# Kernel optimization log

Hardware: AMD Instinct MI355X
Metric: run time of the kernel (lower is better)

The kernel has to match this reference:

```python
import jax, jax.numpy as jnp
import numpy as np

NEG_SLOPE = 0.2  # PyG GATConv default negative_slope
EPS = 1e-16     # PyG softmax denominator epsilon


def gat_layer(x, src, dst, W, att_src, att_dst, bias, N):
    """PyG-style GATConv: gather -> leaky-relu score -> segment softmax -> scatter-add.
    x: [N, F_in], W: [F_in, H*C], att_src/att_dst: [H, C], bias: [H*C].
    src/dst: [E] edge endpoints (messages flow src -> dst), self-loops included.
    """
    H, C = att_src.shape
    h = (x @ W).reshape(N, H, C)                       # [N, H, C]
    a_s = jnp.sum(h * att_src, axis=-1)                # [N, H]
    a_d = jnp.sum(h * att_dst, axis=-1)                # [N, H]
    e = a_s[src] + a_d[dst]                            # [E, H]
    e = jnp.where(e > 0, e, NEG_SLOPE * e)             # leaky relu
    m = jax.ops.segment_max(e, dst, num_segments=N)    # [N, H] (self-loops ensure every node hit)
    p = jnp.exp(e - m[dst])                            # [E, H]
    s = jax.ops.segment_sum(p, dst, num_segments=N)    # [N, H]
    alpha = p / (s[dst] + EPS)                         # [E, H]
    out = jax.ops.segment_sum(alpha[:, :, None] * h[src], dst, num_segments=N)  # [N, H, C]
    return out.reshape(N, H * C) + bias


def setup_inputs() -> dict:
    key = jax.random.key(0)
    ks = jax.random.split(key, 12)
    N, E = 100000, 1600000
    x = jax.random.normal(ks[0], (N, 1), dtype=jnp.float32)
    edge_index = jax.random.randint(ks[1], (2, E), 0, N, dtype=jnp.int32)
    sc = 0.1
    # conv1: in=1, heads=4, out=8
    W1 = jax.random.normal(ks[2], (1, 32), dtype=jnp.float32) * sc
    att_src1 = jax.random.normal(ks[3], (4, 8), dtype=jnp.float32) * sc
    att_dst1 = jax.random.normal(ks[4], (4, 8), dtype=jnp.float32) * sc
    bias1 = jnp.zeros((32,), dtype=jnp.float32)
    # conv2: in=32, heads=8, out=8
    W2 = jax.random.normal(ks[5], (32, 64), dtype=jnp.float32) * sc
    att_src2 = jax.random.normal(ks[6], (8, 8), dtype=jnp.float32) * sc
    att_dst2 = jax.random.normal(ks[7], (8, 8), dtype=jnp.float32) * sc
    bias2 = jnp.zeros((64,), dtype=jnp.float32)
    # fc2: 64 -> 1
    fc_w = jax.random.normal(ks[8], (64, 1), dtype=jnp.float32) * sc
    fc_b = jnp.zeros((1,), dtype=jnp.float32)
    return {"x": x, "edge_index": edge_index,
            "W1": W1, "att_src1": att_src1, "att_dst1": att_dst1, "bias1": bias1,
            "W2": W2, "att_src2": att_src2, "att_dst2": att_dst2, "bias2": bias2,
            "fc_w": fc_w, "fc_b": fc_b}


def reference(x, edge_index, W1, att_src1, att_dst1, bias1,
              W2, att_src2, att_dst2, bias2, fc_w, fc_b):
    N = x.shape[0]
    loop = jnp.arange(N, dtype=edge_index.dtype)       # add_self_loops=True (PyG default)
    src = jnp.concatenate([edge_index[0], loop])
    dst = jnp.concatenate([edge_index[1], loop])
    h = jax.nn.elu(gat_layer(x, src, dst, W1, att_src1, att_dst1, bias1, N))
    h = jax.nn.elu(gat_layer(h, src, dst, W2, att_src2, att_dst2, bias2, N))
    return h @ fc_w + fc_b                             # [N, 1]
```

## Files before the change

kernel.cpp:

```cpp
#include <hip/hip_runtime.h>
#include <hip/hip_fp16.h>
#include <cmath>

#define TPB 256
#define STPB 512
#define NSLOPE 0.2f
#define SEPS 1e-16f

#define BSH 7
#define BNODES 128
#define NBMAX 1024
#define NCHUNK2 256
#define SCTPB 1024
#define CAP 32
#define STAGE 4608
#define MAXDEG 96

__device__ __forceinline__ float lrelu(float v) { return v > 0.f ? v : NSLOPE * v; }
__device__ __forceinline__ float elu1(float v)  { return v > 0.f ? v : expm1f(v); }
__device__ __forceinline__ float elu1f(float v) { return v > 0.f ? v : __expf(v) - 1.f; }

__global__ void k_bscatter(const int* __restrict__ srcI, const int* __restrict__ dstI,
                           int E, int NB, int chunk,
                           int* __restrict__ pk, unsigned char* __restrict__ cnt8) {
    __shared__ int cntL[NBMAX];
    int t = threadIdx.x;
    int c = blockIdx.x;
    int beg = c * chunk;
    int end = min(beg + chunk, E);
    for (int i = t; i < NBMAX; i += SCTPB) cntL[i] = 0;
    __syncthreads();
    for (int e = beg + t; e < end; e += SCTPB) {
        int s = srcI[e], d = dstI[e];
        int b = d >> BSH;
        int r = atomicAdd(&cntL[b], 1);
        if (r < CAP)
            pk[((size_t)b * NCHUNK2 + c) * CAP + r] = (s << BSH) | (d & (BNODES - 1));
    }
    __syncthreads();
    for (int i = t; i < NB; i += SCTPB)
        cnt8[(size_t)i * NCHUNK2 + c] = (unsigned char)min(cntL[i], CAP);
}

__global__ void k_sl1h2(const int* __restrict__ pk, const unsigned char* __restrict__ cnt8,
                        unsigned cap,
                        const float* __restrict__ x,
                        const float* __restrict__ as1, const float* __restrict__ ad1,
                        const float* __restrict__ W1, const float* __restrict__ b1,
                        const float* __restrict__ W2, const float* __restrict__ attS,
                        const float* __restrict__ attD, int N,
                        unsigned* __restrict__ offsets, int* __restrict__ sortedSrc,
                        __half* __restrict__ h2h, float* __restrict__ aS, float* __restrict__ aD) {
    __shared__ __align__(16) char upool[BNODES * 36 * 4];
    int* praw = (int*)upool;
    float (*lds1)[36] = (float (*)[36])upool;
    __shared__ int sorted[STAGE];
    __shared__ int cnt[BNODES];
    __shared__ int offl[BNODES];
    __shared__ int scnt[NCHUNK2];
    __shared__ int sbase[NCHUNK2];
    __shared__ float SDs[8];
    __shared__ int wt4[4], wo4[4];
    __shared__ int mTot, w0tot;
    int b = blockIdx.x, t = threadIdx.x;
    int lane = t & 63, wv = t >> 6;
    int base = b << BSH;
    unsigned rbeg = (unsigned)b * cap;
    if (t < BNODES) cnt[t] = (base + t < N) ? 1 : 0;
    if (t < 8) {
        int h = t & 3;
        const float* att = (t >= 4) ? ad1 : as1;
        float acc = 0.f;
        #pragma unroll
        for (int cc = 0; cc < 8; ++cc) acc += W1[h*8+cc] * att[h*8+cc];
        SDs[t] = acc;
    }
    int myc = (t < NCHUNK2) ? (int)cnt8[(size_t)b * NCHUNK2 + t] : 0;
    int inc2 = myc;
    #pragma unroll
    for (int off = 1; off < 64; off <<= 1) {
        int u = __shfl_up(inc2, off);
        if (lane >= off) inc2 += u;
    }
    if (t < NCHUNK2 && lane == 63) wt4[wv] = inc2;
    __syncthreads();
    if (t < 4) {
        int xv = wt4[t];
        int sc_ = xv;
        #pragma unroll
        for (int off = 1; off < 4; off <<= 1) {
            int u = __shfl_up(sc_, off);
            if (t >= off) sc_ += u;
        }
        wo4[t] = sc_ - xv;
        if (t == 3) mTot = sc_;
    }
    __syncthreads();
    if (t < NCHUNK2) {
        scnt[t] = myc;
        sbase[t] = inc2 + wo4[wv] - myc;
    }
    __syncthreads();
    {
        const int4* slab = (const int4*)(pk + (size_t)b * NCHUNK2 * CAP);
        for (int i4 = t; i4 < NCHUNK2 * CAP / 4; i4 += STPB) {
            int4 v = slab[i4];
            int c = i4 >> 3;
            int j0 = (i4 & 7) << 2;
            int cv = scnt[c];
            if (j0 < cv) {
                int sb = sbase[c];
                int nv = min(4, cv - j0);
                int vv0 = v.x, vv1 = v.y, vv2 = v.z, vv3 = v.w;
                if (0 < nv && sb + j0 + 0 < STAGE) { praw[sb + j0 + 0] = vv0; atomicAdd(&cnt[vv0 & (BNODES - 1)], 1); }
                if (1 < nv && sb + j0 + 1 < STAGE) { praw[sb + j0 + 1] = vv1; atomicAdd(&cnt[vv1 & (BNODES - 1)], 1); }
                if (2 < nv && sb + j0 + 2 < STAGE) { praw[sb + j0 + 2] = vv2; atomicAdd(&cnt[vv2 & (BNODES - 1)], 1); }
                if (3 < nv && sb + j0 + 3 < STAGE) { praw[sb + j0 + 3] = vv3; atomicAdd(&cnt[vv3 & (BNODES - 1)], 1); }
            }
        }
        if (t < BNODES && base + t < N && mTot + t < STAGE)
            praw[mTot + t] = ((base + t) << BSH) | t;
    }
    __syncthreads();
    int m = min(mTot + min(BNODES, N - base), STAGE);
    int v = (t < BNODES) ? cnt[t] : 0;
    int inc = v;
    #pragma unroll
    for (int off = 1; off < 64; off <<= 1) {
        int u = __shfl_up(inc, off);
        if (lane >= off) inc += u;
    }
    if (t == 63) w0tot = inc;
    __syncthreads();
    if (t >= 64 && t < BNODES) inc += w0tot;
    if (t < BNODES) {
        int ex = inc - v;
        int d = base + t;
        if (d < N) offsets[d] = ((rbeg + (unsigned)ex) << 10) | (unsigned)v;
        cnt[t] = 0;
        offl[t] = ex;
    }
    __syncthreads();
    for (int i = t; i < m; i += STPB) {
        int p = praw[i];
        int dl = p & (BNODES - 1);
        int r = atomicAdd(&cnt[dl], 1);
        sorted[offl[dl] + r] = p >> BSH;
    }
    __syncthreads();
    for (int i = t; i < m; i += STPB) sortedSrc[rbeg + i] = sorted[i];
    __syncthreads();
    int n = t >> 2, q = t & 3;
    int d2 = base + n;
    bool active = (d2 < N);
    float s0 = 0.f, s1 = 0.f, s2 = 0.f, s3 = 0.f;
    float g0 = 0.f, g1 = 0.f, g2 = 0.f, g3 = 0.f;
    if (active) {
        int deg = cnt[n];
        int lbeg = offl[n];
        float xd = x[d2];
        float S0 = SDs[0], S1 = SDs[1], S2 = SDs[2], S3 = SDs[3];
        float D0 = xd*SDs[4], D1 = xd*SDs[5], D2 = xd*SDs[6], D3 = xd*SDs[7];
        int dq = (deg + 3) >> 2;
        int i = lbeg + q * dq;
        int rem = min(dq, deg - q * dq);
        for (; rem >= 2; rem -= 2, i += 2) {
            int a0 = sorted[i];
            int a1 = sorted[i + 1];
            float x0 = x[a0], x1 = x[a1];
            float p;
            p = __expf(lrelu(x0*S0 + D0)); s0 += p; g0 += p * x0;
            p = __expf(lrelu(x0*S1 + D1)); s1 += p; g1 += p * x0;
            p = __expf(lrelu(x0*S2 + D2)); s2 += p; g2 += p * x0;
            p = __expf(lrelu(x0*S3 + D3)); s3 += p; g3 += p * x0;
            p = __expf(lrelu(x1*S0 + D0)); s0 += p; g0 += p * x1;
            p = __expf(lrelu(x1*S1 + D1)); s1 += p; g1 += p * x1;
            p = __expf(lrelu(x1*S2 + D2)); s2 += p; g2 += p * x1;
            p = __expf(lrelu(x1*S3 + D3)); s3 += p; g3 += p * x1;
        }
        if (rem > 0) {
            int a0 = sorted[i];
            float xs = x[a0];
            float p;
            p = __expf(lrelu(xs*S0 + D0)); s0 += p; g0 += p * xs;
            p = __expf(lrelu(xs*S1 + D1)); s1 += p; g1 += p * xs;
            p = __expf(lrelu(xs*S2 + D2)); s2 += p; g2 += p * xs;
            p = __expf(lrelu(xs*S3 + D3)); s3 += p; g3 += p * xs;
        }
    }
    s0 += __shfl_xor(s0, 1); s1 += __shfl_xor(s1, 1);
    s2 += __shfl_xor(s2, 1); s3 += __shfl_xor(s3, 1);
    g0 += __shfl_xor(g0, 1); g1 += __shfl_xor(g1, 1);
    g2 += __shfl_xor(g2, 1); g3 += __shfl_xor(g3, 1);
    s0 += __shfl_xor(s0, 2); s1 += __shfl_xor(s1, 2);
    s2 += __shfl_xor(s2, 2); s3 += __shfl_xor(s3, 2);
    g0 += __shfl_xor(g0, 2); g1 += __shfl_xor(g1, 2);
    g2 += __shfl_xor(g2, 2); g3 += __shfl_xor(g3, 2);
    if (active) {
        float gq = (q == 0) ? g0 / (s0 + SEPS) :
                   (q == 1) ? g1 / (s1 + SEPS) :
                   (q == 2) ? g2 / (s2 + SEPS) :
                              g3 / (s3 + SEPS);
        #pragma unroll
        for (int cc = 0; cc < 8; ++cc)
            lds1[n][q*8+cc] = elu1(gq * W1[q*8+cc] + b1[q*8+cc]);
    }
    __syncthreads();
    int sub = t >> 6;
    float w2r[32];
    #pragma unroll
    for (int k = 0; k < 32; ++k) w2r[k] = W2[k*64 + lane];
    float attSl = attS[lane], attDl = attD[lane];
    int nCnt = min(BNODES, N - base);
    for (int nn = sub; nn < nCnt; nn += 8) {
        const float4* row4 = (const float4*)lds1[nn];
        float acc = 0.f;
        #pragma unroll
        for (int k4 = 0; k4 < 8; ++k4) {
            float4 rv = row4[k4];
            acc += rv.x*w2r[4*k4] + rv.y*w2r[4*k4+1] + rv.z*w2r[4*k4+2] + rv.w*w2r[4*k4+3];
        }
        int node = base + nn;
        h2h[(size_t)node*64 + lane] = __float2half(acc);
        float ps = acc * attSl;
        float pd = acc * attDl;
        #pragma unroll
        for (int mm = 1; mm < 8; mm <<= 1) {
            ps += __shfl_xor(ps, mm);
            pd += __shfl_xor(pd, mm);
        }
        int hh = lane >> 3, cc = lane & 7;
        if (cc == 0) aS[(size_t)node*8 + hh] = ps;
        if (cc == 1) aD[(size_t)node*8 + hh] = pd;
    }
}

__global__ void k_agg(const unsigned* __restrict__ offsets, const int* __restrict__ ss,
                      const float* __restrict__ aS, const float* __restrict__ aD,
                      const __half* __restrict__ h2h, const float* __restrict__ b2,
                      const float* __restrict__ fcw, const float* __restrict__ fcb,
                      float* __restrict__ out, int N) {
    __shared__ int sl[4][MAXDEG];
    int lane = threadIdx.x & 63;
    int w = threadIdx.x >> 6;
    int d = blockIdx.x * 4 + w;
    if (d >= N) return;
    unsigned u = offsets[d];
    unsigned beg = u >> 10;
    int deg = (int)(u & 1023u);
    int lH   = lane & 31;
    int half = lane >> 5;
    int hh   = lH >> 2;
    const __half2* __restrict__ hp = (const __half2*)h2h;
    float sum = 0.f, ax = 0.f, ay = 0.f;
    if (deg <= MAXDEG) {
        int degPad = (deg + 7) & ~7;
        for (int j = lane; j < degPad; j += 64) sl[w][j] = ss[beg + (unsigned)min(j, deg - 1)];
        float adv = aD[(unsigned)d * 8u + (unsigned)hh];
        for (int e = 0; e < degPad; e += 8) {
            int bi = e + half;
            int s0 = sl[w][bi],     s1 = sl[w][bi + 2];
            int s2 = sl[w][bi + 4], s3 = sl[w][bi + 6];
            float a0 = aS[(unsigned)s0 * 8u + (unsigned)hh];
            float a1 = aS[(unsigned)s1 * 8u + (unsigned)hh];
            float a2 = aS[(unsigned)s2 * 8u + (unsigned)hh];
            float a3 = aS[(unsigned)s3 * 8u + (unsigned)hh];
            float2 g0 = __half22float2(hp[(unsigned)s0 * 32u + (unsigned)lH]);
            float2 g1 = __half22float2(hp[(unsigned)s1 * 32u + (unsigned)lH]);
            float2 g2 = __half22float2(hp[(unsigned)s2 * 32u + (unsigned)lH]);
            float2 g3 = __half22float2(hp[(unsigned)s3 * 32u + (unsigned)lH]);
            float p0 = __expf(lrelu(a0 + adv));
            float p1 = __expf(lrelu(a1 + adv));
            float p2 = __expf(lrelu(a2 + adv));
            float p3 = __expf(lrelu(a3 + adv));
            if (e + 8 > deg) {
                if (bi     >= deg) p0 = 0.f;
                if (bi + 2 >= deg) p1 = 0.f;
                if (bi + 4 >= deg) p2 = 0.f;
                if (bi + 6 >= deg) p3 = 0.f;
            }
            ax += p0*g0.x + p1*g1.x + p2*g2.x + p3*g3.x;
            ay += p0*g0.y + p1*g1.y + p2*g2.y + p3*g3.y;
            sum += (p0 + p1) + (p2 + p3);
        }
    } else {
        float adh = aD[(size_t)d*8 + hh];
        for (int e = half; e < deg; e += 2) {
            int s = ss[beg + e];
            float p = __expf(lrelu(aS[(size_t)s*8 + hh] + adh));
            float2 g = __half22float2(*(const __half2*)(h2h + (size_t)s*64 + 2*lH));
            ax += p*g.x; ay += p*g.y; sum += p;
        }
    }
    ax  += __shfl_xor(ax, 32);
    ay  += __shfl_xor(ay, 32);
    sum += __shfl_xor(sum, 32);
    float inv = 1.f / (sum + SEPS);
    float tt = elu1f(ax*inv + b2[2*lH]) * fcw[2*lH]
             + elu1f(ay*inv + b2[2*lH+1]) * fcw[2*lH+1];
    #pragma unroll
    for (int m = 16; m; m >>= 1) tt += __shfl_xor(tt, m);
    if (lane == 0) out[d] = tt + fcb[0];
}

extern "C" void kernel_launch(void* const* d_in, const int* in_sizes, int n_in,
                              void* d_out, int out_size, void* d_ws, size_t ws_size,
                              hipStream_t stream) {
    const float* x    = (const float*)d_in[0];
    const int*   ei   = (const int*)  d_in[1];
    const float* W1   = (const float*)d_in[2];
    const float* as1  = (const float*)d_in[3];
    const float* ad1  = (const float*)d_in[4];
    const float* b1   = (const float*)d_in[5];
    const float* W2   = (const float*)d_in[6];
    const float* attS2= (const float*)d_in[7];
    const float* attD2= (const float*)d_in[8];
    const float* b2   = (const float*)d_in[9];
    const float* fcw  = (const float*)d_in[10];
    const float* fcb  = (const float*)d_in[11];
    float* out = (float*)d_out;

    int N = in_sizes[0];
    int E = in_sizes[1] / 2;
    int ET = E + N;
    int NB = (N + BNODES - 1) / BNODES;
    unsigned cap = (unsigned)((ET + NB - 1) / NB + 512);
    cap = (cap + 3u) & ~3u;

    const int* srcI = ei;
    const int* dstI = ei + E;

    float* ws = (float*)d_ws;
    size_t off = 0;
    int*      pk        = (int*)(ws + off); off += (size_t)NB * NCHUNK2 * CAP;
    unsigned char* cnt8 = (unsigned char*)(ws + off); off += ((size_t)NB * NCHUNK2 + 3) / 4;
    unsigned* offsets   = (unsigned*)(ws + off); off += (size_t)N + 16;
    int*      sortedSrc = (int*)(ws + off); off += (size_t)NB * cap;
    float*    aS2       = ws + off; off += (size_t)N * 8;
    float*    aD2       = ws + off; off += (size_t)N * 8;
    off = (off + 31) & ~(size_t)31;
    __half*   h2h       = (__half*)(ws + off); off += (size_t)N * 32;

    int chunk = (E + NCHUNK2 - 1) / NCHUNK2;
    k_bscatter<<<NCHUNK2, SCTPB, 0, stream>>>(srcI, dstI, E, NB, chunk, pk, cnt8);
    k_sl1h2   <<<NB, STPB, 0, stream>>>(pk, cnt8, cap, x, as1, ad1, W1, b1,
                                        W2, attS2, attD2,
                                        N, offsets, sortedSrc, h2h, aS2, aD2);
    k_agg     <<<(N + 3) / 4, TPB, 0, stream>>>(offsets, sortedSrc, aS2, aD2, h2h,
                                                b2, fcw, fcb, out, N);
}
```

Before: 188.0 us.

## Split fused sort and layer-1/h2 kernel into separate sort and compute kernels

The fused bucket-sort plus layer-1 aggregation plus h2 projection kernel becomes two kernels. k_sort builds offsets and the sorted source list. k_l1h2 then reads them back from global memory, with 64 nodes per 256-thread block. The split aims to shrink the large LDS footprint and register pressure so the compute phase reaches higher occupancy and more blocks. The cost is an extra launch and a global round trip of sortedSrc instead of reading it from LDS.

```diff
diff --git a/kernel.cpp b/kernel.cpp
--- a/kernel.cpp
+++ b/kernel.cpp
@@ -14,6 +14,7 @@
 #define SCTPB 1024
 #define CAP 32
 #define STAGE 4608
+#define LNODES 64
 #define MAXDEG 96
 
 __device__ __forceinline__ float lrelu(float v) { return v > 0.f ? v : NSLOPE * v; }
@@ -42,24 +43,15 @@
         cnt8[(size_t)i * NCHUNK2 + c] = (unsigned char)min(cntL[i], CAP);
 }
 
-__global__ void k_sl1h2(const int* __restrict__ pk, const unsigned char* __restrict__ cnt8,
-                        unsigned cap,
-                        const float* __restrict__ x,
-                        const float* __restrict__ as1, const float* __restrict__ ad1,
-                        const float* __restrict__ W1, const float* __restrict__ b1,
-                        const float* __restrict__ W2, const float* __restrict__ attS,
-                        const float* __restrict__ attD, int N,
-                        unsigned* __restrict__ offsets, int* __restrict__ sortedSrc,
-                        __half* __restrict__ h2h, float* __restrict__ aS, float* __restrict__ aD) {
-    __shared__ __align__(16) char upool[BNODES * 36 * 4];
-    int* praw = (int*)upool;
-    float (*lds1)[36] = (float (*)[36])upool;
+__global__ void k_sort(const int* __restrict__ pk, const unsigned char* __restrict__ cnt8,
+                       unsigned cap, int N,
+                       unsigned* __restrict__ offsets, int* __restrict__ sortedSrc) {
+    __shared__ int praw[STAGE];
     __shared__ int sorted[STAGE];
     __shared__ int cnt[BNODES];
     __shared__ int offl[BNODES];
     __shared__ int scnt[NCHUNK2];
     __shared__ int sbase[NCHUNK2];
-    __shared__ float SDs[8];
     __shared__ int wt4[4], wo4[4];
     __shared__ int mTot, w0tot;
     int b = blockIdx.x, t = threadIdx.x;
@@ -67,14 +59,6 @@
     int base = b << BSH;
     unsigned rbeg = (unsigned)b * cap;
     if (t < BNODES) cnt[t] = (base + t < N) ? 1 : 0;
-    if (t < 8) {
-        int h = t & 3;
-        const float* att = (t >= 4) ? ad1 : as1;
-        float acc = 0.f;
-        #pragma unroll
-        for (int cc = 0; cc < 8; ++cc) acc += W1[h*8+cc] * att[h*8+cc];
-        SDs[t] = acc;
-    }
     int myc = (t < NCHUNK2) ? (int)cnt8[(size_t)b * NCHUNK2 + t] : 0;
     int inc2 = myc;
     #pragma unroll
@@ -149,6 +133,27 @@
     }
     __syncthreads();
     for (int i = t; i < m; i += STPB) sortedSrc[rbeg + i] = sorted[i];
+}
+
+__global__ void k_l1h2(const unsigned* __restrict__ offsets, const int* __restrict__ ss,
+                       const float* __restrict__ x,
+                       const float* __restrict__ as1, const float* __restrict__ ad1,
+                       const float* __restrict__ W1, const float* __restrict__ b1,
+                       const float* __restrict__ W2, const float* __restrict__ attS,
+                       const float* __restrict__ attD, int N,
+                       __half* __restrict__ h2h, float* __restrict__ aS, float* __restrict__ aD) {
+    __shared__ float lds1[LNODES][36];
+    __shared__ float SDs[8];
+    int t = threadIdx.x;
+    int base = blockIdx.x * LNODES;
+    if (t < 8) {
+        int h = t & 3;
+        const float* att = (t >= 4) ? ad1 : as1;
+        float acc = 0.f;
+        #pragma unroll
+        for (int cc = 0; cc < 8; ++cc) acc += W1[h*8+cc] * att[h*8+cc];
+        SDs[t] = acc;
+    }
     __syncthreads();
     int n = t >> 2, q = t & 3;
     int d2 = base + n;
@@ -156,17 +161,18 @@
     float s0 = 0.f, s1 = 0.f, s2 = 0.f, s3 = 0.f;
     float g0 = 0.f, g1 = 0.f, g2 = 0.f, g3 = 0.f;
     if (active) {
-        int deg = cnt[n];
-        int lbeg = offl[n];
+        unsigned u = offsets[d2];
+        unsigned beg = u >> 10;
+        int deg = (int)(u & 1023u);
         float xd = x[d2];
         float S0 = SDs[0], S1 = SDs[1], S2 = SDs[2], S3 = SDs[3];
         float D0 = xd*SDs[4], D1 = xd*SDs[5], D2 = xd*SDs[6], D3 = xd*SDs[7];
         int dq = (deg + 3) >> 2;
-        int i = lbeg + q * dq;
+        int i = q * dq;
         int rem = min(dq, deg - q * dq);
         for (; rem >= 2; rem -= 2, i += 2) {
-            int a0 = sorted[i];
-            int a1 = sorted[i + 1];
+            int a0 = ss[beg + (unsigned)i];
+            int a1 = ss[beg + (unsigned)(i + 1)];
             float x0 = x[a0], x1 = x[a1];
             float p;
             p = __expf(lrelu(x0*S0 + D0)); s0 += p; g0 += p * x0;
@@ -179,7 +185,7 @@
             p = __expf(lrelu(x1*S3 + D3)); s3 += p; g3 += p * x1;
         }
         if (rem > 0) {
-            int a0 = sorted[i];
+            int a0 = ss[beg + (unsigned)i];
             float xs = x[a0];
             float p;
             p = __expf(lrelu(xs*S0 + D0)); s0 += p; g0 += p * xs;
@@ -206,13 +212,14 @@
             lds1[n][q*8+cc] = elu1(gq * W1[q*8+cc] + b1[q*8+cc]);
     }
     __syncthreads();
+    int lane = t & 63;
     int sub = t >> 6;
     float w2r[32];
     #pragma unroll
     for (int k = 0; k < 32; ++k) w2r[k] = W2[k*64 + lane];
     float attSl = attS[lane], attDl = attD[lane];
-    int nCnt = min(BNODES, N - base);
-    for (int nn = sub; nn < nCnt; nn += 8) {
+    int nCnt = min(LNODES, N - base);
+    for (int nn = sub; nn < nCnt; nn += 4) {
         const float4* row4 = (const float4*)lds1[nn];
         float acc = 0.f;
         #pragma unroll
@@ -343,9 +350,10 @@
 
     int chunk = (E + NCHUNK2 - 1) / NCHUNK2;
     k_bscatter<<<NCHUNK2, SCTPB, 0, stream>>>(srcI, dstI, E, NB, chunk, pk, cnt8);
-    k_sl1h2   <<<NB, STPB, 0, stream>>>(pk, cnt8, cap, x, as1, ad1, W1, b1,
-                                        W2, attS2, attD2,
-                                        N, offsets, sortedSrc, h2h, aS2, aD2);
+    k_sort    <<<NB, STPB, 0, stream>>>(pk, cnt8, cap, N, offsets, sortedSrc);
+    k_l1h2    <<<(N + LNODES - 1) / LNODES, TPB, 0, stream>>>(offsets, sortedSrc, x,
+                                        as1, ad1, W1, b1, W2, attS2, attD2,
+                                        N, h2h, aS2, aD2);
     k_agg     <<<(N + 3) / 4, TPB, 0, stream>>>(offsets, sortedSrc, aS2, aD2, h2h,
                                                 b2, fcw, fcb, out, N);
 }
```

Result: no change. 186.8 us (-0.6%).
